# Performance work log

Hardware: AMD Instinct MI355X
Metric: run time of the kernel (lower is better)

The kernel has to match this reference:

```python
import jax, jax.numpy as jnp
import numpy as np
import math

B, H, LQ, LK, D = 2, 16, 2048, 2048, 128

def setup_inputs() -> dict:
    key = jax.random.key(0)
    kq, kk, kv, km = jax.random.split(key, 4)
    return {
        "query": jax.random.normal(kq, (B, H, LQ, D), dtype=jnp.float32),
        "key": jax.random.normal(kk, (B, H, LK, D), dtype=jnp.float32),
        "value": jax.random.normal(kv, (B, H, LK, D), dtype=jnp.float32),
        # positive integer multiplicities in [1, 8] so log() is finite
        "key_multiplicities": jax.random.randint(km, (B, LK), 1, 9, dtype=jnp.int32),
    }

def reference(query, key, value, key_multiplicities):
    scale = 1.0 / math.sqrt(query.shape[-1])
    # scores: [B, H, Lq, Lk]
    scores = jnp.einsum("bhqd,bhkd->bhqk", query, key) * scale
    # additive log-multiplicity bias, broadcast over heads and queries
    log_mult = jnp.log(key_multiplicities.astype(scores.dtype))  # [B, Lk]
    scores = scores + log_mult[:, None, None, :]
    attn = jax.nn.softmax(scores, axis=-1)
    # dropout_p = 0.0 -> identity
    return jnp.einsum("bhqk,bhkd->bhqd", attn, value)
```

## Files before the change

kernel.cpp:

```cpp
#include <hip/hip_runtime.h>
#include <hip/hip_bf16.h>

constexpr int B_  = 2;
constexpr int H_  = 16;
constexpr int LQ_ = 2048;
constexpr int LK_ = 2048;
constexpr int D_  = 128;

constexpr int BM = 128;
constexpr int BN = 64;
constexpr int NT = LK_ / BN;
constexpr int TILE_SH = 64 * 128;

constexpr float SCALE_LOG2E = 0.12751649734586414f;
constexpr float DEFER_THR   = 8.0f;

typedef short s16x8 __attribute__((ext_vector_type(8)));
typedef float f32x16 __attribute__((ext_vector_type(16)));

#define MFMA32 __builtin_amdgcn_mfma_f32_32x32x16_bf16

#if __has_builtin(__builtin_amdgcn_exp2f)
#define EXP2(x) __builtin_amdgcn_exp2f(x)
#else
#define EXP2(x) exp2f(x)
#endif
#if __has_builtin(__builtin_amdgcn_logf)
#define LOG2(x) __builtin_amdgcn_logf(x)
#else
#define LOG2(x) log2f(x)
#endif

static __device__ __forceinline__ int pk2bf(float a, float b) {
  float2 t{a, b};
  __hip_bfloat162 h = __float22bfloat162_rn(t);
  return *reinterpret_cast<int*>(&h);
}

static __device__ __forceinline__ void dma16(const short* g, short* l) {
  __builtin_amdgcn_global_load_lds(
      (const __attribute__((address_space(1))) void*)g,
      (__attribute__((address_space(3))) void*)l, 16, 0, 0);
}

__global__ __launch_bounds__(256)
void prep(const float* __restrict__ kg, const float* __restrict__ vg,
          const int* __restrict__ multg, short* __restrict__ wsK,
          short* __restrict__ wsV, float* __restrict__ wsBias) {
  __shared__ float tileF[64 * 133];
  const int tid = threadIdx.x;
  const int wg  = blockIdx.x;
  const float* kp = kg + (size_t)wg * 64 * 128;
  const float* vp = vg + (size_t)wg * 64 * 128;
  short* wk = wsK + (size_t)wg * TILE_SH;
  short* wv = wsV + (size_t)wg * TILE_SH;

#pragma unroll
  for (int i = 0; i < 4; ++i) {
    int idx = tid + i * 256;
    int row = idx >> 4, blk = idx & 15;
    const float* src = kp + row * 128 + blk * 8;
    float4 a = *(const float4*)src;
    float4 c4 = *(const float4*)(src + 4);
    int4 t;
    t.x = pk2bf(a.x, a.y);  t.y = pk2bf(a.z, a.w);
    t.z = pk2bf(c4.x, c4.y); t.w = pk2bf(c4.z, c4.w);
    int pos = blk ^ (row & 15);
    *(int4*)&wk[row * 128 + pos * 8] = t;
  }

#pragma unroll
  for (int i = 0; i < 8; ++i) {
    int idx = tid + i * 256;
    int key = idx >> 5, d0 = (idx & 31) * 4;
    float4 a = *(const float4*)(vp + key * 128 + d0);
    float* dst = &tileF[key * 133 + d0];
    dst[0] = a.x; dst[1] = a.y; dst[2] = a.z; dst[3] = a.w;
  }
  __syncthreads();
#pragma unroll
  for (int i = 0; i < 4; ++i) {
    int idx = tid + i * 256;
    int d = idx >> 3, kgrp = idx & 7;
    float v[8];
#pragma unroll
    for (int j = 0; j < 8; ++j) v[j] = tileF[(kgrp * 8 + j) * 133 + d];
    int4 t;
    t.x = pk2bf(v[0], v[1]); t.y = pk2bf(v[2], v[3]);
    t.z = pk2bf(v[4], v[5]); t.w = pk2bf(v[6], v[7]);
    int pos = kgrp ^ ((d >> 1) & 7);
    *(int4*)&wv[d * 64 + pos * 8] = t;
  }

  if (wg < 8) {
    int b = wg >> 2;
    for (int j = tid; j < 512; j += 256) {
      int i0 = (wg & 3) * 512 + j;
      wsBias[b * LK_ + i0] = LOG2((float)multg[b * LK_ + i0]);
    }
  }
}

__global__ __launch_bounds__(256, 2)
void attn_fwd(const float* __restrict__ qg, const short* __restrict__ wsK,
              const short* __restrict__ wsV, const float* __restrict__ wsBias,
              float* __restrict__ outg) {
  __shared__ alignas(16) short Kbuf[2][TILE_SH];
  __shared__ alignas(16) short Vbuf[2][TILE_SH];

  const int tid  = threadIdx.x;
  const int w    = tid >> 6;
  const int lane = tid & 63;
  const int lq   = lane & 31;
  const int hi   = lane >> 5;

  const int L   = blockIdx.y * gridDim.x + blockIdx.x;
  const int k8  = L >> 3;
  const int qb  = k8 & 15;
  const int bh  = (L & 7) * 4 + (k8 >> 4);
  const int b   = bh >> 4;

  const float* qptr = qg + (size_t)bh * LQ_ * D_;
  float*       optr = outg + (size_t)bh * LQ_ * D_;
  const short* kws  = wsK + (size_t)bh * NT * TILE_SH;
  const short* vws  = wsV + (size_t)bh * NT * TILE_SH;
  const float* bias = wsBias + b * LK_;

  const int q0 = qb * BM + w * 32;

  s16x8 qf[8];
  {
    const float* qrow = qptr + (size_t)(q0 + lq) * D_ + hi * 8;
#pragma unroll
    for (int kf = 0; kf < 8; ++kf) {
      float4 a = *(const float4*)(qrow + kf * 16);
      float4 c = *(const float4*)(qrow + kf * 16 + 4);
      int4 t;
      t.x = pk2bf(a.x * SCALE_LOG2E, a.y * SCALE_LOG2E);
      t.y = pk2bf(a.z * SCALE_LOG2E, a.w * SCALE_LOG2E);
      t.z = pk2bf(c.x * SCALE_LOG2E, c.y * SCALE_LOG2E);
      t.w = pk2bf(c.z * SCALE_LOG2E, c.w * SCALE_LOG2E);
      qf[kf] = *(s16x8*)&t;
    }
  }

  f32x16 o[4];
#pragma unroll
  for (int dt = 0; dt < 4; ++dt)
#pragma unroll
    for (int r = 0; r < 16; ++r) o[dt][r] = 0.f;
  float m_r = -INFINITY, l_r = 0.f;

  auto dmaKV = [&](int kt, int bb) {
    const short* gK = kws + (size_t)kt * TILE_SH;
    const short* gV = vws + (size_t)kt * TILE_SH;
#pragma unroll
    for (int i = 0; i < 4; ++i) {
      int off = (w * 4 + i) * 512;
      dma16(gK + off + lane * 8, &Kbuf[bb][off]);
      dma16(gV + off + lane * 8, &Vbuf[bb][off]);
    }
  };

  dmaKV(0, 0);
  __syncthreads();

  for (int kt = 0; kt < NT; ++kt) {
    const int cur = kt & 1;
    if (kt + 1 < NT) dmaKV(kt + 1, cur ^ 1);

    f32x16 St[2];
#pragma unroll
    for (int t = 0; t < 2; ++t)
#pragma unroll
      for (int g = 0; g < 4; ++g) {
        float4 bv = *(const float4*)&bias[kt * BN + t * 32 + g * 8 + hi * 4];
        St[t][g * 4 + 0] = bv.x; St[t][g * 4 + 1] = bv.y;
        St[t][g * 4 + 2] = bv.z; St[t][g * 4 + 3] = bv.w;
      }

    __builtin_amdgcn_s_setprio(1);
#pragma unroll
    for (int t = 0; t < 2; ++t) {
      const short* kb = &Kbuf[cur][(t * 32 + lq) * 128];
#pragma unroll
      for (int kf = 0; kf < 8; ++kf) {
        s16x8 kfr = *(const s16x8*)&kb[((2 * kf + hi) ^ (lq & 15)) * 8];
        St[t] = MFMA32(kfr, qf[kf], St[t], 0, 0, 0);
      }
    }
    __builtin_amdgcn_s_setprio(0);

    float t16[16];
#pragma unroll
    for (int i = 0; i < 16; ++i) t16[i] = fmaxf(St[0][i], St[1][i]);
#pragma unroll
    for (int s = 8; s >= 1; s >>= 1)
#pragma unroll
      for (int i = 0; i < s; ++i) t16[i] = fmaxf(t16[i], t16[i + s]);
    float mx = fmaxf(t16[0], __shfl_xor(t16[0], 32));

    if (__any(mx - m_r > DEFER_THR)) {
      float mn    = fmaxf(m_r, mx);
      float alpha = EXP2(m_r - mn);
      m_r = mn;
      l_r *= alpha;
      float ar[16];
#pragma unroll
      for (int r = 0; r < 16; ++r)
        ar[r] = __shfl(alpha, (r & 3) + 8 * (r >> 2) + 4 * hi);
#pragma unroll
      for (int dt = 0; dt < 4; ++dt)
#pragma unroll
        for (int r = 0; r < 16; ++r) o[dt][r] *= ar[r];
    }

    float px[2][16];
#pragma unroll
    for (int t = 0; t < 2; ++t)
#pragma unroll
      for (int r = 0; r < 16; ++r) px[t][r] = EXP2(St[t][r] - m_r);

    float sa[16];
#pragma unroll
    for (int i = 0; i < 16; ++i) sa[i] = px[0][i] + px[1][i];
#pragma unroll
    for (int s = 8; s >= 1; s >>= 1)
#pragma unroll
      for (int i = 0; i < s; ++i) sa[i] += sa[i + s];
    l_r += sa[0] + __shfl_xor(sa[0], 32);

    s16x8 pf[2][2];
#pragma unroll
    for (int t = 0; t < 2; ++t) {
      int P[8];
#pragma unroll
      for (int i = 0; i < 8; ++i) P[i] = pk2bf(px[t][2 * i], px[t][2 * i + 1]);
#pragma unroll
      for (int ks = 0; ks < 2; ++ks) {
        int a0 = P[4 * ks + 0], a1 = P[4 * ks + 1];
        int b0 = P[4 * ks + 2], b1 = P[4 * ks + 3];
        asm("v_permlane32_swap_b32 %0, %1" : "+v"(a0), "+v"(b0));
        asm("v_permlane32_swap_b32 %0, %1" : "+v"(a1), "+v"(b1));
        int4 tt{a0, a1, b0, b1};
        pf[t][ks] = *(s16x8*)&tt;
      }
    }

    __builtin_amdgcn_s_setprio(1);
#pragma unroll
    for (int dt = 0; dt < 4; ++dt) {
      const short* vb = &Vbuf[cur][(dt * 32 + lq) * 64];
#pragma unroll
      for (int t = 0; t < 2; ++t)
#pragma unroll
        for (int ks = 0; ks < 2; ++ks) {
          s16x8 vf = *(const s16x8*)
              &vb[((t * 4 + ks * 2 + hi) ^ ((lq >> 1) & 7)) * 8];
          o[dt] = MFMA32(pf[t][ks], vf, o[dt], 0, 0, 0);
        }
    }
    __builtin_amdgcn_s_setprio(0);

    __syncthreads();
  }

  float li[16];
#pragma unroll
  for (int r = 0; r < 16; ++r)
    li[r] = 1.0f / __shfl(l_r, (r & 3) + 8 * (r >> 2) + 4 * hi);
#pragma unroll
  for (int dt = 0; dt < 4; ++dt)
#pragma unroll
    for (int r = 0; r < 16; ++r) {
      int row = q0 + (r & 3) + 8 * (r >> 2) + 4 * hi;
      optr[(size_t)row * D_ + dt * 32 + lq] = o[dt][r] * li[r];
    }
}

extern "C" void kernel_launch(void* const* d_in, const int* in_sizes, int n_in,
                              void* d_out, int out_size, void* d_ws, size_t ws_size,
                              hipStream_t stream) {
  const float* q = (const float*)d_in[0];
  const float* k = (const float*)d_in[1];
  const float* v = (const float*)d_in[2];
  const int* mult = (const int*)d_in[3];
  float* out = (float*)d_out;

  constexpr size_t KV_BYTES = (size_t)B_ * H_ * LK_ * D_ * 2;
  short* wsK = (short*)d_ws;
  short* wsV = (short*)((char*)d_ws + KV_BYTES);
  float* wsBias = (float*)((char*)d_ws + 2 * KV_BYTES);

  prep<<<dim3(B_ * H_ * NT), dim3(256), 0, stream>>>(k, v, mult, wsK, wsV, wsBias);

  dim3 grid(LQ_ / BM, B_ * H_);
  attn_fwd<<<grid, dim3(256), 0, stream>>>(q, wsK, wsV, wsBias, out);
}
```

Before: 213.9 us.

## Single-buffer V tile with split waits to raise occupancy to three blocks

Drops the V double buffer, so shared memory per block goes from 64KB to 48KB, and raises launch bounds to 3 blocks per CU. V for the current tile is now loaded at the start of each iteration, with a partial vmcnt wait and barrier placed before the PV MFMAs. The next K tile is still prefetched into a double buffer. This trades V load latency that is less hidden, plus an extra barrier per iteration, for more resident waves. It also reuses the score registers for the exponentials to reduce register pressure.

Measured after the change: 228.0 us. 1.07x slower.

```diff
diff --git a/kernel.cpp b/kernel.cpp
--- a/kernel.cpp
+++ b/kernel.cpp
@@ -101,12 +101,12 @@
   }
 }
 
-__global__ __launch_bounds__(256, 2)
+__global__ __launch_bounds__(256, 3)
 void attn_fwd(const float* __restrict__ qg, const short* __restrict__ wsK,
               const short* __restrict__ wsV, const float* __restrict__ wsBias,
               float* __restrict__ outg) {
   __shared__ alignas(16) short Kbuf[2][TILE_SH];
-  __shared__ alignas(16) short Vbuf[2][TILE_SH];
+  __shared__ alignas(16) short Vbuf[TILE_SH];
 
   const int tid  = threadIdx.x;
   const int w    = tid >> 6;
@@ -151,23 +151,32 @@
     for (int r = 0; r < 16; ++r) o[dt][r] = 0.f;
   float m_r = -INFINITY, l_r = 0.f;
 
-  auto dmaKV = [&](int kt, int bb) {
+  auto dmaK = [&](int kt, int bb) {
     const short* gK = kws + (size_t)kt * TILE_SH;
-    const short* gV = vws + (size_t)kt * TILE_SH;
 #pragma unroll
     for (int i = 0; i < 4; ++i) {
       int off = (w * 4 + i) * 512;
       dma16(gK + off + lane * 8, &Kbuf[bb][off]);
-      dma16(gV + off + lane * 8, &Vbuf[bb][off]);
     }
   };
-
-  dmaKV(0, 0);
-  __syncthreads();
+  auto dmaV = [&](int kt) {
+    const short* gV = vws + (size_t)kt * TILE_SH;
+#pragma unroll
+    for (int i = 0; i < 4; ++i) {
+      int off = (w * 4 + i) * 512;
+      dma16(gV + off + lane * 8, &Vbuf[off]);
+    }
+  };
+
+  dmaK(0, 0);
+  asm volatile("s_waitcnt vmcnt(0)" ::: "memory");
+  __builtin_amdgcn_s_barrier();
+  __builtin_amdgcn_sched_barrier(0);
 
   for (int kt = 0; kt < NT; ++kt) {
     const int cur = kt & 1;
-    if (kt + 1 < NT) dmaKV(kt + 1, cur ^ 1);
+    dmaV(kt);
+    if (kt + 1 < NT) dmaK(kt + 1, cur ^ 1);
 
     f32x16 St[2];
 #pragma unroll
@@ -215,15 +224,14 @@
         for (int r = 0; r < 16; ++r) o[dt][r] *= ar[r];
     }
 
-    float px[2][16];
 #pragma unroll
     for (int t = 0; t < 2; ++t)
 #pragma unroll
-      for (int r = 0; r < 16; ++r) px[t][r] = EXP2(St[t][r] - m_r);
+      for (int r = 0; r < 16; ++r) St[t][r] = EXP2(St[t][r] - m_r);
 
     float sa[16];
 #pragma unroll
-    for (int i = 0; i < 16; ++i) sa[i] = px[0][i] + px[1][i];
+    for (int i = 0; i < 16; ++i) sa[i] = St[0][i] + St[1][i];
 #pragma unroll
     for (int s = 8; s >= 1; s >>= 1)
 #pragma unroll
@@ -235,7 +243,7 @@
     for (int t = 0; t < 2; ++t) {
       int P[8];
 #pragma unroll
-      for (int i = 0; i < 8; ++i) P[i] = pk2bf(px[t][2 * i], px[t][2 * i + 1]);
+      for (int i = 0; i < 8; ++i) P[i] = pk2bf(St[t][2 * i], St[t][2 * i + 1]);
 #pragma unroll
       for (int ks = 0; ks < 2; ++ks) {
         int a0 = P[4 * ks + 0], a1 = P[4 * ks + 1];
@@ -247,10 +255,18 @@
       }
     }
 
+    if (kt + 1 < NT) {
+      asm volatile("s_waitcnt vmcnt(4)" ::: "memory");
+    } else {
+      asm volatile("s_waitcnt vmcnt(0)" ::: "memory");
+    }
+    __builtin_amdgcn_s_barrier();
+    __builtin_amdgcn_sched_barrier(0);
+
     __builtin_amdgcn_s_setprio(1);
 #pragma unroll
     for (int dt = 0; dt < 4; ++dt) {
-      const short* vb = &Vbuf[cur][(dt * 32 + lq) * 64];
+      const short* vb = &Vbuf[(dt * 32 + lq) * 64];
 #pragma unroll
       for (int t = 0; t < 2; ++t)
 #pragma unroll
@@ -262,7 +278,11 @@
     }
     __builtin_amdgcn_s_setprio(0);
 
-    __syncthreads();
+    if (kt + 1 < NT) {
+      asm volatile("s_waitcnt vmcnt(0)" ::: "memory");
+      __builtin_amdgcn_s_barrier();
+      __builtin_amdgcn_sched_barrier(0);
+    }
   }
 
   float li[16];
```

## Software-pipeline QK^T of next tile with softmax/PV of current tile

Applied to the files above, without the earlier changes.

Restructures the main loop so the QK^T MFMAs for tile t+1 are issued before the softmax and PV work of tile t. Two score register sets alternate between iterations. K loads now run two tiles ahead and V loads one tile ahead, with one barrier per iteration at the top. The per-batch bias row is also staged once into LDS instead of being read from global memory every tile. This aims to overlap MFMA work with exp and reduction work, at the cost of more VGPRs and about 8KB more LDS per block, which could hurt occupancy.

Result: faster. 208.9 us (-2.3%).

```diff
diff --git a/kernel.cpp b/kernel.cpp
--- a/kernel.cpp
+++ b/kernel.cpp
@@ -107,6 +107,7 @@
               float* __restrict__ outg) {
   __shared__ alignas(16) short Kbuf[2][TILE_SH];
   __shared__ alignas(16) short Vbuf[2][TILE_SH];
+  __shared__ alignas(16) float biasLds[LK_];
 
   const int tid  = threadIdx.x;
   const int w    = tid >> 6;
@@ -127,6 +128,14 @@
   const float* bias = wsBias + b * LK_;
 
   const int q0 = qb * BM + w * 32;
+
+  {
+    int i = tid * 8;
+    float4 a = *(const float4*)&bias[i];
+    float4 c = *(const float4*)&bias[i + 4];
+    *(float4*)&biasLds[i] = a;
+    *(float4*)&biasLds[i + 4] = c;
+  }
 
   s16x8 qf[8];
   {
@@ -151,38 +160,40 @@
     for (int r = 0; r < 16; ++r) o[dt][r] = 0.f;
   float m_r = -INFINITY, l_r = 0.f;
 
-  auto dmaKV = [&](int kt, int bb) {
+  auto dmaK = [&](int kt) {
     const short* gK = kws + (size_t)kt * TILE_SH;
-    const short* gV = vws + (size_t)kt * TILE_SH;
+    short* lb = &Kbuf[kt & 1][0];
 #pragma unroll
     for (int i = 0; i < 4; ++i) {
       int off = (w * 4 + i) * 512;
-      dma16(gK + off + lane * 8, &Kbuf[bb][off]);
-      dma16(gV + off + lane * 8, &Vbuf[bb][off]);
+      dma16(gK + off + lane * 8, lb + off);
     }
   };
-
-  dmaKV(0, 0);
-  __syncthreads();
-
-  for (int kt = 0; kt < NT; ++kt) {
-    const int cur = kt & 1;
-    if (kt + 1 < NT) dmaKV(kt + 1, cur ^ 1);
-
-    f32x16 St[2];
+  auto dmaV = [&](int kt) {
+    const short* gV = vws + (size_t)kt * TILE_SH;
+    short* lb = &Vbuf[kt & 1][0];
+#pragma unroll
+    for (int i = 0; i < 4; ++i) {
+      int off = (w * 4 + i) * 512;
+      dma16(gV + off + lane * 8, lb + off);
+    }
+  };
+
+  auto qk = [&](int kt, f32x16* St) {
+    const float* bl = &biasLds[kt * BN];
 #pragma unroll
     for (int t = 0; t < 2; ++t)
 #pragma unroll
       for (int g = 0; g < 4; ++g) {
-        float4 bv = *(const float4*)&bias[kt * BN + t * 32 + g * 8 + hi * 4];
+        float4 bv = *(const float4*)&bl[t * 32 + g * 8 + hi * 4];
         St[t][g * 4 + 0] = bv.x; St[t][g * 4 + 1] = bv.y;
         St[t][g * 4 + 2] = bv.z; St[t][g * 4 + 3] = bv.w;
       }
-
+    const short* kb0 = &Kbuf[kt & 1][0];
     __builtin_amdgcn_s_setprio(1);
 #pragma unroll
     for (int t = 0; t < 2; ++t) {
-      const short* kb = &Kbuf[cur][(t * 32 + lq) * 128];
+      const short* kb = &kb0[(t * 32 + lq) * 128];
 #pragma unroll
       for (int kf = 0; kf < 8; ++kf) {
         s16x8 kfr = *(const s16x8*)&kb[((2 * kf + hi) ^ (lq & 15)) * 8];
@@ -190,10 +201,19 @@
       }
     }
     __builtin_amdgcn_s_setprio(0);
+  };
+
+  auto body = [&](int t, f32x16* Sc, f32x16* Sn, bool doNext, bool doK) {
+    __syncthreads();
+    if (doNext) dmaV(t + 1);
+    if (doK)    dmaK(t + 2);
+    __builtin_amdgcn_sched_barrier(0);
+
+    if (doNext) qk(t + 1, Sn);
 
     float t16[16];
 #pragma unroll
-    for (int i = 0; i < 16; ++i) t16[i] = fmaxf(St[0][i], St[1][i]);
+    for (int i = 0; i < 16; ++i) t16[i] = fmaxf(Sc[0][i], Sc[1][i]);
 #pragma unroll
     for (int s = 8; s >= 1; s >>= 1)
 #pragma unroll
@@ -215,15 +235,14 @@
         for (int r = 0; r < 16; ++r) o[dt][r] *= ar[r];
     }
 
-    float px[2][16];
-#pragma unroll
-    for (int t = 0; t < 2; ++t)
-#pragma unroll
-      for (int r = 0; r < 16; ++r) px[t][r] = EXP2(St[t][r] - m_r);
+#pragma unroll
+    for (int tt = 0; tt < 2; ++tt)
+#pragma unroll
+      for (int r = 0; r < 16; ++r) Sc[tt][r] = EXP2(Sc[tt][r] - m_r);
 
     float sa[16];
 #pragma unroll
-    for (int i = 0; i < 16; ++i) sa[i] = px[0][i] + px[1][i];
+    for (int i = 0; i < 16; ++i) sa[i] = Sc[0][i] + Sc[1][i];
 #pragma unroll
     for (int s = 8; s >= 1; s >>= 1)
 #pragma unroll
@@ -232,38 +251,50 @@
 
     s16x8 pf[2][2];
 #pragma unroll
-    for (int t = 0; t < 2; ++t) {
+    for (int tt = 0; tt < 2; ++tt) {
       int P[8];
 #pragma unroll
-      for (int i = 0; i < 8; ++i) P[i] = pk2bf(px[t][2 * i], px[t][2 * i + 1]);
+      for (int i = 0; i < 8; ++i) P[i] = pk2bf(Sc[tt][2 * i], Sc[tt][2 * i + 1]);
 #pragma unroll
       for (int ks = 0; ks < 2; ++ks) {
         int a0 = P[4 * ks + 0], a1 = P[4 * ks + 1];
         int b0 = P[4 * ks + 2], b1 = P[4 * ks + 3];
         asm("v_permlane32_swap_b32 %0, %1" : "+v"(a0), "+v"(b0));
         asm("v_permlane32_swap_b32 %0, %1" : "+v"(a1), "+v"(b1));
-        int4 tt{a0, a1, b0, b1};
-        pf[t][ks] = *(s16x8*)&tt;
+        int4 tt2{a0, a1, b0, b1};
+        pf[tt][ks] = *(s16x8*)&tt2;
       }
     }
 
+    const short* vb0 = &Vbuf[t & 1][0];
     __builtin_amdgcn_s_setprio(1);
 #pragma unroll
     for (int dt = 0; dt < 4; ++dt) {
-      const short* vb = &Vbuf[cur][(dt * 32 + lq) * 64];
-#pragma unroll
-      for (int t = 0; t < 2; ++t)
+      const short* vb = &vb0[(dt * 32 + lq) * 64];
+#pragma unroll
+      for (int tt = 0; tt < 2; ++tt)
 #pragma unroll
         for (int ks = 0; ks < 2; ++ks) {
           s16x8 vf = *(const s16x8*)
-              &vb[((t * 4 + ks * 2 + hi) ^ ((lq >> 1) & 7)) * 8];
-          o[dt] = MFMA32(pf[t][ks], vf, o[dt], 0, 0, 0);
+              &vb[((tt * 4 + ks * 2 + hi) ^ ((lq >> 1) & 7)) * 8];
+          o[dt] = MFMA32(pf[tt][ks], vf, o[dt], 0, 0, 0);
         }
     }
     __builtin_amdgcn_s_setprio(0);
-
-    __syncthreads();
-  }
+  };
+
+  dmaK(0); dmaV(0);
+  __syncthreads();
+  dmaK(1);
+  f32x16 StA[2], StB[2];
+  qk(0, StA);
+
+  for (int t = 0; t < NT - 2; t += 2) {
+    body(t,     StA, StB, true, true);
+    body(t + 1, StB, StA, true, true);
+  }
+  body(NT - 2, StA, StB, true,  false);
+  body(NT - 1, StB, StA, false, false);
 
   float li[16];
 #pragma unroll
```
